# Kernel optimization log

Hardware: AMD Instinct MI355X
Metric: run time of the kernel (lower is better)

Reference implementation:

```python
import jax, jax.numpy as jnp
import numpy as np

B, L, D, N, H = 4, 1024, 1024, 16, 64  # batch, seq, d_model, n_head, d_head
R = 2 * L  # relative position table length
EPS = 1e-5


def setup_inputs() -> dict:
    key = jax.random.key(0)
    ks = jax.random.split(key, 16)
    s = D ** -0.5
    q = jax.random.normal(ks[0], (B, L, D), jnp.float32)
    k = jax.random.normal(ks[1], (B, L, D), jnp.float32)
    v = jax.random.normal(ks[2], (B, L, D), jnp.float32)
    pos_encodings = jax.random.normal(ks[3], (R, D), jnp.float32)
    padding = jax.random.randint(ks[4], (B, 1, 1, L), 0, 2).astype(bool)
    q_w = jax.random.normal(ks[5], (D, N, H), jnp.float32) * s
    k_w = jax.random.normal(ks[6], (D, N, H), jnp.float32) * s
    k_b = jnp.zeros((N, H), jnp.float32)
    v_w = jax.random.normal(ks[7], (D, N, H), jnp.float32) * s
    v_b = jnp.zeros((N, H), jnp.float32)
    r_w_bias = jax.random.normal(ks[8], (N, 1, H), jnp.float32) * 0.02
    r_r_bias = jax.random.normal(ks[9], (N, 1, H), jnp.float32) * 0.02
    r_kernel = jax.random.normal(ks[10], (N, D, H), jnp.float32) * s
    post_w = jax.random.normal(ks[11], (N, H, D), jnp.float32) * (N * H) ** -0.5
    post_b = jnp.zeros((D,), jnp.float32)
    ln_g = jnp.ones((D,), jnp.float32)
    ln_b = jnp.zeros((D,), jnp.float32)
    return dict(q=q, k=k, v=v, pos_encodings=pos_encodings, padding=padding,
                q_w=q_w, k_w=k_w, k_b=k_b, v_w=v_w, v_b=v_b,
                r_w_bias=r_w_bias, r_r_bias=r_r_bias, r_kernel=r_kernel,
                post_w=post_w, post_b=post_b, ln_g=ln_g, ln_b=ln_b)


def _funnel_attention(q, k, v, pos_encodings, padding, q_w, k_w, k_b, v_w, v_b,
                      r_w_bias, r_r_bias, r_kernel, post_w, post_b, ln_g, ln_b):
    input_q = q
    d_head = q_w.shape[-1]
    scale = d_head ** -0.5
    # head projections, laid out [b, n, l, h]
    qh = jnp.einsum('bld,dnh->bnlh', q, q_w)
    kh = jnp.einsum('bld,dnh->bnlh', k, k_w) + k_b[None, :, None, :]
    vh = jnp.einsum('bld,dnh->bnlh', v, v_w) + v_b[None, :, None, :]
    # content term with r_w_bias
    attn_score = jnp.einsum('bnlh,bnmh->bnlm', qh + r_w_bias[None], kh) * scale
    # relative-position term (rel_shift)
    r = jnp.einsum('rd,ndh->nrh', pos_encodings, r_kernel)  # [n, R, h]
    pos = jnp.einsum('bnlh,nrh->bnlr', qh + r_r_bias[None], r) * scale  # [b,n,L,R]
    b, n, q_len, r_len = pos.shape
    k_len = kh.shape[-2]
    shift = 1 + (q_len != k_len)
    pos = pos.reshape(b, n, r_len, q_len)
    pos = pos[:, :, shift:, :]
    pos = pos.reshape(b, n, q_len, r_len - shift)[..., :k_len]
    attn_score = attn_score + pos
    # key padding mask
    attn_score = attn_score - 1e6 * padding.astype(attn_score.dtype)
    attn_dist = jax.nn.softmax(attn_score, axis=-1)
    out = jnp.einsum('bnlm,bnmh->bnlh', attn_dist, vh)
    attn_out = jnp.einsum('bnlh,nhd->bld', out, post_w) + post_b
    x = input_q + attn_out
    mu = jnp.mean(x, axis=-1, keepdims=True)
    var = jnp.mean(jnp.square(x - mu), axis=-1, keepdims=True)
    return (x - mu) * jax.lax.rsqrt(var + EPS) * ln_g + ln_b


def reference(q, k, v, pos_encodings, padding, q_w, k_w, k_b, v_w, v_b,
              r_w_bias, r_r_bias, r_kernel, post_w, post_b, ln_g, ln_b):
    return _funnel_attention(q, k, v, pos_encodings, padding, q_w, k_w, k_b,
                             v_w, v_b, r_w_bias, r_r_bias, r_kernel,
                             post_w, post_b, ln_g, ln_b)
```

## Files before the change

kernel.cpp:

```cpp
#include <hip/hip_runtime.h>
#include <hip/hip_bf16.h>

#define Bb 4
#define Ls 1024
#define Dd 1024
#define Nn 16
#define Hh 64
#define Rr 2048

typedef __attribute__((ext_vector_type(8))) short short8;
typedef __attribute__((ext_vector_type(4))) short short4v;
typedef __attribute__((ext_vector_type(4))) float f32x4;

__device__ __forceinline__ float bf2f(short s) {
    union { unsigned u; float f; } c;
    c.u = ((unsigned)(unsigned short)s) << 16;
    return c.f;
}
__device__ __forceinline__ short f2bf(float f) {
    __hip_bfloat16 h = __float2bfloat16(f);
    return *reinterpret_cast<short*>(&h);
}

__device__ __forceinline__ void gld16(const void* g, void* l) {
    __builtin_amdgcn_global_load_lds(
        (const __attribute__((address_space(1))) unsigned int*)g,
        (__attribute__((address_space(3))) unsigned int*)l, 16, 0, 0);
}

struct CopyDesc {
    const float* src[4];
    short* dst[4];
    int n[4];
};

__global__ __launch_bounds__(256) void f2bf_multi(CopyDesc cd) {
    const int z = blockIdx.y;
    const int base = (blockIdx.x * 256 + threadIdx.x) * 8;
    if (base >= cd.n[z]) return;
    const float* s = cd.src[z] + base;
    const float4 a = *(const float4*)s;
    const float4 b = *(const float4*)(s + 4);
    short8 o;
    o[0] = f2bf(a.x); o[1] = f2bf(a.y); o[2] = f2bf(a.z); o[3] = f2bf(a.w);
    o[4] = f2bf(b.x); o[5] = f2bf(b.y); o[6] = f2bf(b.z); o[7] = f2bf(b.w);
    *(short8*)(cd.dst[z] + base) = o;
}

struct TransDesc {
    const float* src[4];
    short* dst[4];
};

__global__ __launch_bounds__(256) void transpose_all(
    TransDesc td, const float* __restrict__ rker, short* __restrict__ rkT)
{
    const int z = blockIdx.z;
    const float* in; short* out; int C, R;
    if (z < 4) {
        in = td.src[z]; out = td.dst[z]; C = 1024; R = 1024;
    } else {
        if (blockIdx.x != 0) return;
        in  = rker + (long)(z - 4) * 1024 * 64;
        out = rkT  + (long)(z - 4) * 64 * 1024;
        C = 64; R = 1024;
    }
    const int r0 = blockIdx.y * 64, c0 = blockIdx.x * 64;
    __shared__ float T[64][65];
    const int t = threadIdx.x;
    const int rr = t >> 4, c4 = (t & 15) * 4;
#pragma unroll
    for (int p = 0; p < 4; ++p) {
        const float4 v = *(const float4*)&in[(long)(r0 + p * 16 + rr) * C + c0 + c4];
        T[p * 16 + rr][c4 + 0] = v.x;
        T[p * 16 + rr][c4 + 1] = v.y;
        T[p * 16 + rr][c4 + 2] = v.z;
        T[p * 16 + rr][c4 + 3] = v.w;
    }
    __syncthreads();
#pragma unroll
    for (int p = 0; p < 4; ++p) {
        const int j = p * 16 + (t >> 4);
        const int d4 = (t & 15) * 4;
        short4v o;
#pragma unroll
        for (int u = 0; u < 4; ++u) o[u] = f2bf(T[d4 + u][j]);
        *(short4v*)&out[(long)(c0 + j) * R + r0 + d4] = o;
    }
}

__global__ __launch_bounds__(256) void gemm_bt(
    const short* __restrict__ A, int lda, long aStride,
    const short* __restrict__ Bt, int ldb, long bStride,
    const float* __restrict__ bias,
    const float* __restrict__ kb, const float* __restrict__ vb,
    const float* __restrict__ residual, int ldr,
    void* __restrict__ Cv, int ldc, long cStride, int out_bf16, int K, int zsplit)
{
    const int bid   = (int)blockIdx.x;
    const int chunk = (int)gridDim.x >> 3;
    const int work  = (bid & 7) * chunk + (bid >> 3);
    int z, r;
    if (work < zsplit) { z = work >> 8; r = work & 255; }
    else               { z = 3;         r = work - zsplit; }
    const int by = r >> 3;
    const int bx = r & 7;

    A  += (long)z * aStride;
    Bt += (long)z * bStride;

    const int row0 = by * 128;
    const int col0 = bx * 128;

    __shared__ short As[2][128 * 32];
    __shared__ short Bs[2][128 * 32];

    const int tid  = threadIdx.x;
    const int w    = tid >> 6;
    const int lane = tid & 63;
    const int quad = lane >> 4;
    const int ln16 = lane & 15;
    const int wr   = (w >> 1) * 64;
    const int wc   = (w & 1) * 64;

    f32x4 acc[4][4];
#pragma unroll
    for (int a = 0; a < 4; ++a)
#pragma unroll
        for (int b = 0; b < 4; ++b) acc[a][b] = (f32x4){0.f, 0.f, 0.f, 0.f};

    const int srow = w * 16 + (lane >> 2);
    const int scol = (lane & 3) * 8;
    const short* gA = A  + (long)(row0 + srow) * lda + scol;
    const short* gB = Bt + (long)(col0 + srow) * ldb + scol;

    gld16(gA,                  As[0] + w * 512);
    gld16(gA + (long)64 * lda, As[0] + w * 512 + 2048);
    gld16(gB,                  Bs[0] + w * 512);
    gld16(gB + (long)64 * ldb, Bs[0] + w * 512 + 2048);
    __syncthreads();

    int cur = 0;
    for (int k0 = 0; k0 < K; k0 += 32) {
        if (k0 + 32 < K) {
            const int nxt = cur ^ 1;
            gld16(gA + k0 + 32,                  As[nxt] + w * 512);
            gld16(gA + k0 + 32 + (long)64 * lda, As[nxt] + w * 512 + 2048);
            gld16(gB + k0 + 32,                  Bs[nxt] + w * 512);
            gld16(gB + k0 + 32 + (long)64 * ldb, Bs[nxt] + w * 512 + 2048);
        }

        short8 af[4], bfr[4];
#pragma unroll
        for (int tm = 0; tm < 4; ++tm)
            af[tm] = *(const short8*)&As[cur][(wr + tm * 16 + ln16) * 32 + quad * 8];
#pragma unroll
        for (int tn = 0; tn < 4; ++tn)
            bfr[tn] = *(const short8*)&Bs[cur][(wc + tn * 16 + ln16) * 32 + quad * 8];
#pragma unroll
        for (int tm = 0; tm < 4; ++tm)
#pragma unroll
            for (int tn = 0; tn < 4; ++tn)
                acc[tm][tn] = __builtin_amdgcn_mfma_f32_16x16x32_bf16(
                    af[tm], bfr[tn], acc[tm][tn], 0, 0, 0);

        __syncthreads();
        cur ^= 1;
    }

    const float* bz = bias;
    if (z == 1) bz = kb;
    else if (z == 2) bz = vb;

    float bv[4];
#pragma unroll
    for (int tn = 0; tn < 4; ++tn)
        bv[tn] = bz ? bz[col0 + wc + tn * 16 + ln16] : 0.f;

    short* Cb = (short*)Cv + (long)z * cStride;
    float* Cf = (float*)Cv + (long)z * cStride;
#pragma unroll
    for (int tm = 0; tm < 4; ++tm) {
#pragma unroll
        for (int r2 = 0; r2 < 4; ++r2) {
            const long row = row0 + wr + tm * 16 + quad * 4 + r2;
#pragma unroll
            for (int tn = 0; tn < 4; ++tn) {
                const int col = col0 + wc + tn * 16 + ln16;
                float val = acc[tm][tn][r2] + bv[tn];
                if (residual) val += residual[row * (long)ldr + col];
                if (out_bf16) Cb[row * (long)ldc + col] = f2bf(val);
                else          Cf[row * (long)ldc + col] = val;
            }
        }
    }
}

#define SCALE_L2E 0.18033688f

__global__ __launch_bounds__(256, 2) void attn_mfma(
    const short* __restrict__ qh, const short* __restrict__ kh,
    const short* __restrict__ vh, const short* __restrict__ rS,
    const int* __restrict__ padding, const float* __restrict__ rwb,
    const float* __restrict__ rrb, short* __restrict__ ao)
{
    const int bid   = (int)blockIdx.x;
    const int chunk = (int)gridDim.x >> 3;
    const int work  = (bid & 7) * chunk + (bid >> 3);
    const int lt = work & 7;
    const int n  = (work >> 3) & 15;
    const int b  = work >> 7;

    const int l0 = lt * 128;
    const int tid  = threadIdx.x;
    const int w    = tid >> 6;
    const int lane = tid & 63;
    const int quad = lane >> 4;
    const int ln16 = lane & 15;
    const int qb   = w * 32;

    __shared__ __align__(16) short ks[64 * 64];
    __shared__ __align__(16) short rsb[256 * 64];
    __shared__ __align__(16) short vsT[64][72];
    __shared__ __align__(16) short psm[4][2][16][72];
    __shared__ unsigned padw[32];

#pragma unroll
    for (int j = 0; j < 4; ++j) {
        const int g = w + 4 * j;
        const unsigned long long m =
            __ballot(padding[b * Ls + g * 64 + lane] != 0);
        if (lane == 0) {
            padw[2 * g]     = (unsigned)m;
            padw[2 * g + 1] = (unsigned)(m >> 32);
        }
    }

    short8 qwf[2][2], qrf[2][2];
#pragma unroll
    for (int qt = 0; qt < 2; ++qt) {
        const long rowoff =
            ((long)(b * Ls + l0 + qb + qt * 16 + ln16)) * (Nn * Hh) + n * Hh;
#pragma unroll
        for (int c = 0; c < 2; ++c) {
            const int kb2 = c * 32 + quad * 8;
            short8 qv = *(const short8*)(qh + rowoff + kb2);
#pragma unroll
            for (int j = 0; j < 8; ++j) {
                float qf = bf2f(qv[j]);
                qwf[qt][c][j] = f2bf(qf + rwb[n * Hh + kb2 + j]);
                qrf[qt][c][j] = f2bf(qf + rrb[n * Hh + kb2 + j]);
            }
        }
    }

    float lsum[2][4];
    f32x4 accO[2][4];
#pragma unroll
    for (int qt = 0; qt < 2; ++qt)
#pragma unroll
        for (int r = 0; r < 4; ++r) {
            lsum[qt][r] = 0.f;
            accO[qt][r] = (f32x4){0.f, 0.f, 0.f, 0.f};
        }

    const int srow8 = lane >> 3;
    const int sunit = (lane & 7) ^ srow8;
    const int swz   = ln16 & 7;

    {
        const int base0 = 897 - l0;
#pragma unroll
        for (int j = 0; j < 6; ++j) {
            const int c = w * 6 + j;
            const int rg = base0 + c * 8 + srow8;
            gld16(rS + (long)rg * 1024 + n * 64 + sunit * 8,
                  rsb + c * 512);
        }
    }

    const int s5  = tid & 31;
    const int kp2 = (s5 & 15) + ((s5 >> 4) << 5);
    const int kcb = 4 * (s5 & 15) + 2 * (s5 >> 4);
    const int cq  = (tid >> 5) * 8;
    short8 va, vb2;
    {
        const short* vp = vh + ((long)(b * Ls + kp2)) * 1024 + n * 64 + cq;
        va  = *(const short8*)vp;
        vb2 = *(const short8*)(vp + 16 * 1024);
    }

    for (int mt = 0; mt < Ls / 64; ++mt) {
        const int m0 = mt * 64;
        __syncthreads();

#pragma unroll
        for (int j = 0; j < 2; ++j) {
            const int c = w * 2 + j;
            gld16(kh + ((long)(b * Ls + m0 + c * 8 + srow8)) * 1024
                     + n * 64 + sunit * 8,
                  ks + c * 512);
        }
        {
            const int tail = 1089 + m0 - l0;
            const int rcB  = (24 + 8 * mt) & 31;
#pragma unroll
            for (int j = 0; j < 2; ++j) {
                const int jl = w * 2 + j;
                const int rc = (rcB + jl) & 31;
                int rg = tail + jl * 8 + srow8;
                rg = rg < 2047 ? rg : 2047;
                gld16(rS + (long)rg * 1024 + n * 64 + sunit * 8,
                      rsb + rc * 512);
            }
        }
#pragma unroll
        for (int u = 0; u < 8; ++u) {
            unsigned pk = ((unsigned)(unsigned short)va[u]) |
                          (((unsigned)(unsigned short)vb2[u]) << 16);
            *(unsigned*)&vsT[cq + u][kcb] = pk;
        }
        __syncthreads();

        {
            const int mn = (m0 + 64) & (Ls - 1);
            const short* vp = vh + ((long)(b * Ls + mn + kp2)) * 1024 + n * 64 + cq;
            va  = *(const short8*)vp;
            vb2 = *(const short8*)(vp + 16 * 1024);
        }

        const int rb0 = (96 - qb) + ln16 + m0;
        short8 rfU[6][2];
#pragma unroll
        for (int s = 0; s < 6; ++s) {
            const int rr2 = (rb0 + s * 16) & 255;
#pragma unroll
            for (int c2 = 0; c2 < 2; ++c2) {
                const int unit = (c2 * 4 + quad) ^ swz;
                rfU[s][c2] = *(const short8*)&rsb[rr2 * 64 + unit * 8];
            }
        }

        __builtin_amdgcn_s_setprio(1);
        f32x4 Sf[2][4];
#pragma unroll
        for (int t = 0; t < 4; ++t) {
            short8 kf0, kf1;
            {
                const int u0 = (0 * 4 + quad) ^ swz;
                const int u1 = (1 * 4 + quad) ^ swz;
                kf0 = *(const short8*)&ks[(t * 16 + ln16) * 64 + u0 * 8];
                kf1 = *(const short8*)&ks[(t * 16 + ln16) * 64 + u1 * 8];
            }
#pragma unroll
            for (int qt = 0; qt < 2; ++qt) {
                f32x4 c = (f32x4){0.f, 0.f, 0.f, 0.f};
                c = __builtin_amdgcn_mfma_f32_16x16x32_bf16(qwf[qt][0], kf0, c, 0, 0, 0);
                c = __builtin_amdgcn_mfma_f32_16x16x32_bf16(qwf[qt][1], kf1, c, 0, 0, 0);
                Sf[qt][t] = c;
            }
        }
        f32x4 Prf[2][5];
#pragma unroll
        for (int t = 0; t < 5; ++t) {
#pragma unroll
            for (int qt = 0; qt < 2; ++qt) {
                const int off = qt ? 0 : 1;
                f32x4 c = (f32x4){0.f, 0.f, 0.f, 0.f};
                c = __builtin_amdgcn_mfma_f32_16x16x32_bf16(qrf[qt][0], rfU[t + off][0], c, 0, 0, 0);
                c = __builtin_amdgcn_mfma_f32_16x16x32_bf16(qrf[qt][1], rfU[t + off][1], c, 0, 0, 0);
                Prf[qt][t] = c;
            }
        }
        __builtin_amdgcn_s_setprio(0);

        const unsigned w0 = padw[(m0 >> 5)];
        const unsigned w1 = padw[(m0 >> 5) + 1];
        const float mbc = -16.0f * 1.44269504f;
        const float mb0 = ((w0 >> ln16) & 1)        ? -1.0e7f : mbc;
        const float mb1 = ((w0 >> (16 + ln16)) & 1) ? -1.0e7f : mbc;
        const float mb2 = ((w1 >> ln16) & 1)        ? -1.0e7f : mbc;
        const float mb3 = ((w1 >> (16 + ln16)) & 1) ? -1.0e7f : mbc;
#pragma unroll
        for (int qt = 0; qt < 2; ++qt) {
#pragma unroll
            for (int r = 0; r < 4; ++r) {
                const int row = quad * 4 + r;
                const int u = ln16 - row + 15;
                const int srcLane = (quad << 4) | (u & 15);
                const float s0 = __shfl(Prf[qt][0][r], srcLane, 64);
                const float s1 = __shfl(Prf[qt][1][r], srcLane, 64);
                const float s2 = __shfl(Prf[qt][2][r], srcLane, 64);
                const float s3 = __shfl(Prf[qt][3][r], srcLane, 64);
                const float s4 = __shfl(Prf[qt][4][r], srcLane, 64);
                const bool hi = (u >= 16);
                const float p0 = __builtin_amdgcn_exp2f(
                    fmaf(Sf[qt][0][r] + (hi ? s1 : s0), SCALE_L2E, mb0));
                const float p1 = __builtin_amdgcn_exp2f(
                    fmaf(Sf[qt][1][r] + (hi ? s2 : s1), SCALE_L2E, mb1));
                const float p2 = __builtin_amdgcn_exp2f(
                    fmaf(Sf[qt][2][r] + (hi ? s3 : s2), SCALE_L2E, mb2));
                const float p3 = __builtin_amdgcn_exp2f(
                    fmaf(Sf[qt][3][r] + (hi ? s4 : s3), SCALE_L2E, mb3));
                lsum[qt][r] += (p0 + p1) + (p2 + p3);
                short4v pk;
                pk[0] = f2bf(p0); pk[1] = f2bf(p1);
                pk[2] = f2bf(p2); pk[3] = f2bf(p3);
                *(short4v*)&psm[w][qt][row][ln16 * 4] = pk;
            }
        }

        short8 pA[2][2];
#pragma unroll
        for (int qt = 0; qt < 2; ++qt)
#pragma unroll
            for (int c2 = 0; c2 < 2; ++c2)
                pA[qt][c2] = *(short8*)&psm[w][qt][ln16][c2 * 32 + quad * 8];
        __builtin_amdgcn_s_setprio(1);
#pragma unroll
        for (int t = 0; t < 4; ++t) {
            short8 vf0 = *(short8*)&vsT[t * 16 + ln16][quad * 8];
            short8 vf1 = *(short8*)&vsT[t * 16 + ln16][32 + quad * 8];
#pragma unroll
            for (int qt = 0; qt < 2; ++qt) {
                f32x4 c = accO[qt][t];
                c = __builtin_amdgcn_mfma_f32_16x16x32_bf16(pA[qt][0], vf0, c, 0, 0, 0);
                c = __builtin_amdgcn_mfma_f32_16x16x32_bf16(pA[qt][1], vf1, c, 0, 0, 0);
                accO[qt][t] = c;
            }
        }
        __builtin_amdgcn_s_setprio(0);
    }

#pragma unroll
    for (int qt = 0; qt < 2; ++qt) {
#pragma unroll
        for (int r = 0; r < 4; ++r) {
            float v = lsum[qt][r];
#pragma unroll
            for (int of = 1; of < 16; of <<= 1) v += __shfl_xor(v, of, 64);
            lsum[qt][r] = 1.f / v;
        }
#pragma unroll
        for (int t = 0; t < 4; ++t)
#pragma unroll
            for (int r = 0; r < 4; ++r)
                psm[w][qt][quad * 4 + r][t * 16 + ln16] =
                    f2bf(accO[qt][t][r] * lsum[qt][(unsigned)r]);
#pragma unroll
        for (int p = 0; p < 2; ++p) {
            const int c = lane + p * 64;
            const int row = c >> 3, cq2 = (c & 7) * 8;
            const long grow = (long)(b * Ls + l0 + qb + qt * 16 + row);
            *(short8*)(ao + grow * 1024 + n * 64 + cq2) = *(short8*)&psm[w][qt][row][cq2];
        }
    }
}

__global__ __launch_bounds__(256) void ln_kernel(
    float* x, const float* __restrict__ g, const float* __restrict__ bb)
{
    const int row = blockIdx.x;
    const int tid = threadIdx.x;
    float4 v = ((const float4*)(x + (long)row * Dd))[tid];
    float s  = v.x + v.y + v.z + v.w;
    float sq = v.x * v.x + v.y * v.y + v.z * v.z + v.w * v.w;
#pragma unroll
    for (int off = 32; off; off >>= 1) {
        s  += __shfl_down(s, off, 64);
        sq += __shfl_down(sq, off, 64);
    }
    __shared__ float ws_s[4], ws_q[4];
    __shared__ float s_mu, s_rstd;
    const int wave = tid >> 6, lane = tid & 63;
    if (lane == 0) { ws_s[wave] = s; ws_q[wave] = sq; }
    __syncthreads();
    if (tid == 0) {
        const float ts = ws_s[0] + ws_s[1] + ws_s[2] + ws_s[3];
        const float tq = ws_q[0] + ws_q[1] + ws_q[2] + ws_q[3];
        const float mu = ts / (float)Dd;
        const float var = tq / (float)Dd - mu * mu;
        s_mu = mu;
        s_rstd = rsqrtf(var + 1e-5f);
    }
    __syncthreads();
    const float mu = s_mu, rstd = s_rstd;
    const float4 gv = ((const float4*)g)[tid];
    const float4 bv = ((const float4*)bb)[tid];
    float4 o;
    o.x = (v.x - mu) * rstd * gv.x + bv.x;
    o.y = (v.y - mu) * rstd * gv.y + bv.y;
    o.z = (v.z - mu) * rstd * gv.z + bv.z;
    o.w = (v.w - mu) * rstd * gv.w + bv.w;
    ((float4*)(x + (long)row * Dd))[tid] = o;
}

extern "C" void kernel_launch(void* const* d_in, const int* in_sizes, int n_in,
                              void* d_out, int out_size, void* d_ws, size_t ws_size,
                              hipStream_t stream) {
    const float* q      = (const float*)d_in[0];
    const float* k      = (const float*)d_in[1];
    const float* v      = (const float*)d_in[2];
    const float* posenc = (const float*)d_in[3];
    const int*   pad    = (const int*)  d_in[4];
    const float* q_w    = (const float*)d_in[5];
    const float* k_w    = (const float*)d_in[6];
    const float* k_b    = (const float*)d_in[7];
    const float* v_w    = (const float*)d_in[8];
    const float* v_b    = (const float*)d_in[9];
    const float* rwb    = (const float*)d_in[10];
    const float* rrb    = (const float*)d_in[11];
    const float* r_ker  = (const float*)d_in[12];
    const float* post_w = (const float*)d_in[13];
    const float* post_b = (const float*)d_in[14];
    const float* ln_g   = (const float*)d_in[15];
    const float* ln_b   = (const float*)d_in[16];
    float* out = (float*)d_out;

    const long M1 = 1L << 20;
    short* ws = (short*)d_ws;
    short* xq   = ws;
    short* xk   = ws + 4 * M1;
    short* xv   = ws + 8 * M1;
    short* pe   = ws + 12 * M1;
    short* wT   = ws + 14 * M1;
    short* rkT  = ws + 17 * M1;
    short* pwT  = ws + 18 * M1;
    short* qh   = ws + 19 * M1;
    short* kh   = ws + 23 * M1;
    short* vh   = ws + 27 * M1;
    short* rS   = ws + 31 * M1;
    short* ao   = xq;

    const dim3 blk(256);

    CopyDesc cd;
    cd.src[0] = q;      cd.dst[0] = xq;  cd.n[0] = 4 * (int)M1;
    cd.src[1] = k;      cd.dst[1] = xk;  cd.n[1] = 4 * (int)M1;
    cd.src[2] = v;      cd.dst[2] = xv;  cd.n[2] = 4 * (int)M1;
    cd.src[3] = posenc; cd.dst[3] = pe;  cd.n[3] = 2 * (int)M1;
    f2bf_multi<<<dim3(2048, 4), blk, 0, stream>>>(cd);

    TransDesc td;
    td.src[0] = q_w;    td.dst[0] = wT;
    td.src[1] = k_w;    td.dst[1] = wT + M1;
    td.src[2] = v_w;    td.dst[2] = wT + 2 * M1;
    td.src[3] = post_w; td.dst[3] = pwT;
    transpose_all<<<dim3(16, 16, 20), blk, 0, stream>>>(td, r_ker, rkT);

    gemm_bt<<<dim3(896), blk, 0, stream>>>(
        xq, 1024, 4 * M1, wT, 1024, M1, nullptr, k_b, v_b,
        nullptr, 0, qh, 1024, 4 * M1, 1, 1024, 768);

    attn_mfma<<<dim3(512), blk, 0, stream>>>(
        qh, kh, vh, rS, pad, rwb, rrb, ao);

    gemm_bt<<<dim3(256), blk, 0, stream>>>(
        ao, 1024, 0, pwT, 1024, 0, post_b, nullptr, nullptr,
        q, 1024, out, 1024, 0, 0, 1024, 1 << 30);

    ln_kernel<<<dim3(Bb * Ls), blk, 0, stream>>>(out, ln_g, ln_b);
}
```

Baseline: 301.5 us.

## Merge prep kernels and overlap GEMM prefetch with explicit vmcnt waits

Fuses the fp32-to-bf16 conversion and the weight-transpose kernels into a single prep_all launch with a flat block index, which saves one launch and the blocks that used to exit early in the old transpose grid. The GEMM main loop swaps its end-of-iteration __syncthreads for a barrier at the top plus an explicit s_waitcnt vmcnt(4) after issuing the next tile's async LDS loads. This lets the next tile's loads stay in flight while the current tile is consumed, instead of draining every load. It relies on precise vmcnt accounting and on sched_barrier to keep the compiler from reordering, so miscounting would risk a race.

```diff
diff --git a/kernel.cpp b/kernel.cpp
--- a/kernel.cpp
+++ b/kernel.cpp
@@ -33,41 +33,46 @@
     short* dst[4];
     int n[4];
 };
-
-__global__ __launch_bounds__(256) void f2bf_multi(CopyDesc cd) {
-    const int z = blockIdx.y;
-    const int base = (blockIdx.x * 256 + threadIdx.x) * 8;
-    if (base >= cd.n[z]) return;
-    const float* s = cd.src[z] + base;
-    const float4 a = *(const float4*)s;
-    const float4 b = *(const float4*)(s + 4);
-    short8 o;
-    o[0] = f2bf(a.x); o[1] = f2bf(a.y); o[2] = f2bf(a.z); o[3] = f2bf(a.w);
-    o[4] = f2bf(b.x); o[5] = f2bf(b.y); o[6] = f2bf(b.z); o[7] = f2bf(b.w);
-    *(short8*)(cd.dst[z] + base) = o;
-}
-
 struct TransDesc {
     const float* src[4];
     short* dst[4];
 };
 
-__global__ __launch_bounds__(256) void transpose_all(
-    TransDesc td, const float* __restrict__ rker, short* __restrict__ rkT)
+__global__ __launch_bounds__(256) void prep_all(
+    CopyDesc cd, TransDesc td, const float* __restrict__ rker,
+    short* __restrict__ rkT)
 {
-    const int z = blockIdx.z;
-    const float* in; short* out; int C, R;
-    if (z < 4) {
-        in = td.src[z]; out = td.dst[z]; C = 1024; R = 1024;
+    const int bid = (int)blockIdx.x;
+    const int t   = threadIdx.x;
+
+    if (bid < 8192) {
+        const int z = bid >> 11;
+        const int base = ((bid & 2047) * 256 + t) * 8;
+        if (base >= cd.n[z]) return;
+        const float* s = cd.src[z] + base;
+        const float4 a = *(const float4*)s;
+        const float4 b = *(const float4*)(s + 4);
+        short8 o;
+        o[0] = f2bf(a.x); o[1] = f2bf(a.y); o[2] = f2bf(a.z); o[3] = f2bf(a.w);
+        o[4] = f2bf(b.x); o[5] = f2bf(b.y); o[6] = f2bf(b.z); o[7] = f2bf(b.w);
+        *(short8*)(cd.dst[z] + base) = o;
+        return;
+    }
+
+    const int tw = bid - 8192;
+    const float* in; short* out; int C, r0, c0;
+    if (tw < 1024) {
+        const int z = tw >> 8, rem = tw & 255;
+        in = td.src[z]; out = td.dst[z]; C = 1024;
+        r0 = ((rem >> 4) & 15) * 64; c0 = (rem & 15) * 64;
     } else {
-        if (blockIdx.x != 0) return;
-        in  = rker + (long)(z - 4) * 1024 * 64;
-        out = rkT  + (long)(z - 4) * 64 * 1024;
-        C = 64; R = 1024;
-    }
-    const int r0 = blockIdx.y * 64, c0 = blockIdx.x * 64;
+        const int s2 = tw - 1024;
+        const int sl = s2 >> 4, y = s2 & 15;
+        in  = rker + (long)sl * 1024 * 64;
+        out = rkT  + (long)sl * 64 * 1024;
+        C = 64; r0 = y * 64; c0 = 0;
+    }
     __shared__ float T[64][65];
-    const int t = threadIdx.x;
     const int rr = t >> 4, c4 = (t & 15) * 4;
 #pragma unroll
     for (int p = 0; p < 4; ++p) {
@@ -85,7 +90,7 @@
         short4v o;
 #pragma unroll
         for (int u = 0; u < 4; ++u) o[u] = f2bf(T[d4 + u][j]);
-        *(short4v*)&out[(long)(c0 + j) * R + r0 + d4] = o;
+        *(short4v*)&out[(long)(c0 + j) * 1024 + r0 + d4] = o;
     }
 }
 
@@ -138,17 +143,23 @@
     gld16(gA + (long)64 * lda, As[0] + w * 512 + 2048);
     gld16(gB,                  Bs[0] + w * 512);
     gld16(gB + (long)64 * ldb, Bs[0] + w * 512 + 2048);
-    __syncthreads();
 
     int cur = 0;
     for (int k0 = 0; k0 < K; k0 += 32) {
+        __builtin_amdgcn_s_barrier();
+
         if (k0 + 32 < K) {
             const int nxt = cur ^ 1;
             gld16(gA + k0 + 32,                  As[nxt] + w * 512);
             gld16(gA + k0 + 32 + (long)64 * lda, As[nxt] + w * 512 + 2048);
             gld16(gB + k0 + 32,                  Bs[nxt] + w * 512);
             gld16(gB + k0 + 32 + (long)64 * ldb, Bs[nxt] + w * 512 + 2048);
-        }
+            asm volatile("s_waitcnt vmcnt(4)" ::: "memory");
+        } else {
+            asm volatile("s_waitcnt vmcnt(0)" ::: "memory");
+        }
+        __builtin_amdgcn_s_barrier();
+        __builtin_amdgcn_sched_barrier(0);
 
         short8 af[4], bfr[4];
 #pragma unroll
@@ -164,7 +175,6 @@
                 acc[tm][tn] = __builtin_amdgcn_mfma_f32_16x16x32_bf16(
                     af[tm], bfr[tn], acc[tm][tn], 0, 0, 0);
 
-        __syncthreads();
         cur ^= 1;
     }
 
@@ -539,14 +549,12 @@
     cd.src[1] = k;      cd.dst[1] = xk;  cd.n[1] = 4 * (int)M1;
     cd.src[2] = v;      cd.dst[2] = xv;  cd.n[2] = 4 * (int)M1;
     cd.src[3] = posenc; cd.dst[3] = pe;  cd.n[3] = 2 * (int)M1;
-    f2bf_multi<<<dim3(2048, 4), blk, 0, stream>>>(cd);
-
     TransDesc td;
     td.src[0] = q_w;    td.dst[0] = wT;
     td.src[1] = k_w;    td.dst[1] = wT + M1;
     td.src[2] = v_w;    td.dst[2] = wT + 2 * M1;
     td.src[3] = post_w; td.dst[3] = pwT;
-    transpose_all<<<dim3(16, 16, 20), blk, 0, stream>>>(td, r_ker, rkT);
+    prep_all<<<dim3(9472), blk, 0, stream>>>(cd, td, r_ker, rkT);
 
     gemm_bt<<<dim3(896), blk, 0, stream>>>(
         xq, 1024, 4 * M1, wT, 1024, M1, nullptr, k_b, v_b,
```

Result: faster. 289.3 us (-4.1%).
